# Kernel optimization log

Measured on AMD Instinct MI355X. Metric: run time of the kernel, lower is better.

The kernel has to match this reference:

```python
import jax, jax.numpy as jnp
import numpy as np

# NF4 codebook (16 normal-float levels), same constants as torchao NF4Tensor
NF4_CODEBOOK = jnp.array([
    -1.0, -0.6961928009986877, -0.5250730514526367, -0.39491748809814453,
    -0.28444138169288635, -0.18477343022823334, -0.09105003625154495, 0.0,
    0.07958029955625534, 0.16093020141124725, 0.24611230194568634,
    0.33791524171829224, 0.44070982933044434, 0.5626170039176941,
    0.7229568362236023, 1.0], dtype=jnp.float32)

IN_SIZE = 4096
OUT_SIZE = 12288
BLOCK_SIZE = 64
SCALER_BLOCK_SIZE = 256
EPS = 1e-5


def setup_inputs() -> dict:
    key = jax.random.key(0)
    ks = jax.random.split(key, 7)
    n_blocks = OUT_SIZE * IN_SIZE // BLOCK_SIZE          # 786432
    n_sblocks = n_blocks // SCALER_BLOCK_SIZE            # 3072
    x = jax.random.normal(ks[0], (4096, IN_SIZE), jnp.float32)
    ln_weight = jax.random.uniform(ks[1], (IN_SIZE,), jnp.float32, 0.5, 1.5)
    ln_bias = jax.random.normal(ks[2], (IN_SIZE,), jnp.float32) * 0.02
    codes = jax.random.randint(ks[3], (n_blocks, BLOCK_SIZE), 0, 16, jnp.int32)
    quantized_scalers = jax.random.randint(ks[4], (n_blocks,), 1, 128, jnp.int32)
    quantization_factor = jax.random.uniform(ks[5], (n_sblocks,), jnp.float32, 0.5, 2.0)
    scaler_mean = jax.random.normal(ks[6], (1,), jnp.float32) * 0.01
    return dict(x=x, ln_weight=ln_weight, ln_bias=ln_bias,
                quantization_factor=quantization_factor, scaler_mean=scaler_mean,
                codes=codes, quantized_scalers=quantized_scalers)


def _dequantize_nf4(codes, quantized_scalers, quantization_factor, scaler_mean, in_size):
    # double dequant of per-block scales: int8-range scaler / per-scaler-block factor + mean
    n_blocks = quantized_scalers.shape[0]
    scales = (quantized_scalers.astype(jnp.float32).reshape(-1, SCALER_BLOCK_SIZE)
              / quantization_factor[:, None] + scaler_mean).reshape(n_blocks, 1)
    # codebook lookup + per-block scale, then reshape to [out, in]
    return (NF4_CODEBOOK[codes] * scales).reshape(-1, in_size)


def reference(x, ln_weight, ln_bias, quantization_factor, scaler_mean, codes, quantized_scalers):
    # LayerNorm (eps=1e-5, zero_centered_gamma=False)
    mu = jnp.mean(x, axis=-1, keepdims=True)
    var = jnp.mean(jnp.square(x - mu), axis=-1, keepdims=True)
    ln_out = (x - mu) * jax.lax.rsqrt(var + EPS) * ln_weight + ln_bias
    # NF4 dequant + linear (F.linear: x @ W.T)
    w = _dequantize_nf4(codes, quantized_scalers, quantization_factor, scaler_mean, x.shape[-1])
    linear_out = ln_out @ w.T
    return (linear_out, ln_out)
```

## Files before the change

### kernel.cpp

```cpp
#include <hip/hip_runtime.h>
#include <hip/hip_bf16.h>
#include <stdint.h>

#define IN_SIZE   4096
#define OUT_SIZE  12288
#define M_ROWS    4096
#define LN_EPS    1e-5f
#define N_BLOCKS  786432

typedef __attribute__((ext_vector_type(8))) short bf16x8;
typedef __attribute__((ext_vector_type(4))) float f32x4;

__device__ __constant__ float NF4_CB[16] = {
    -1.0f, -0.6961928009986877f, -0.5250730514526367f, -0.39491748809814453f,
    -0.28444138169288635f, -0.18477343022823334f, -0.09105003625154495f, 0.0f,
    0.07958029955625534f, 0.16093020141124725f, 0.24611230194568634f,
    0.33791524171829224f, 0.44070982933044434f, 0.5626170039176941f,
    0.7229568362236023f, 1.0f };

__device__ __forceinline__ unsigned short f2bf(float f) {
    unsigned u = __builtin_bit_cast(unsigned, f);
    u += 0x7FFFu + ((u >> 16) & 1u);
    return (unsigned short)(u >> 16);
}

__global__ __launch_bounds__(256) void ln_kernel(
    const float* __restrict__ x, const float* __restrict__ gamma,
    const float* __restrict__ beta, float* __restrict__ out_f32,
    unsigned short* __restrict__ out_bf16)
{
    const int row = blockIdx.x;
    const int tid = threadIdx.x;
    const float4* x4 = (const float4*)(x + (size_t)row * IN_SIZE);

    float4 v[4];
    float sum = 0.f, ssq = 0.f;
#pragma unroll
    for (int i = 0; i < 4; ++i) {
        v[i] = x4[tid + i * 256];
        sum += v[i].x + v[i].y + v[i].z + v[i].w;
        ssq += v[i].x * v[i].x + v[i].y * v[i].y + v[i].z * v[i].z + v[i].w * v[i].w;
    }
#pragma unroll
    for (int off = 32; off > 0; off >>= 1) {
        sum += __shfl_down(sum, off, 64);
        ssq += __shfl_down(ssq, off, 64);
    }
    __shared__ float s_sum[4], s_ssq[4];
    const int wave = tid >> 6, lane = tid & 63;
    if (lane == 0) { s_sum[wave] = sum; s_ssq[wave] = ssq; }
    __syncthreads();
    sum = s_sum[0] + s_sum[1] + s_sum[2] + s_sum[3];
    ssq = s_ssq[0] + s_ssq[1] + s_ssq[2] + s_ssq[3];

    const float mu   = sum * (1.f / IN_SIZE);
    const float var  = ssq * (1.f / IN_SIZE) - mu * mu;
    const float rstd = rsqrtf(var + LN_EPS);

    const float4* g4 = (const float4*)gamma;
    const float4* b4 = (const float4*)beta;
    float4* o4 = (float4*)(out_f32 + (size_t)row * IN_SIZE);
    ushort4* ob4 = (ushort4*)(out_bf16 + (size_t)row * IN_SIZE);
#pragma unroll
    for (int i = 0; i < 4; ++i) {
        const int c = tid + i * 256;
        const float4 g = g4[c], b = b4[c];
        float4 y;
        y.x = (v[i].x - mu) * rstd * g.x + b.x;
        y.y = (v[i].y - mu) * rstd * g.y + b.y;
        y.z = (v[i].z - mu) * rstd * g.z + b.z;
        y.w = (v[i].w - mu) * rstd * g.w + b.w;
        o4[c] = y;
        ushort4 p;
        p.x = f2bf(y.x); p.y = f2bf(y.y); p.z = f2bf(y.z); p.w = f2bf(y.w);
        ob4[c] = p;
    }
}

__global__ __launch_bounds__(256) void dq_kernel(
    const int* __restrict__ codes, const int* __restrict__ qs,
    const float* __restrict__ qf, const float* __restrict__ smean,
    unsigned short* __restrict__ wout)
{
    __shared__ float cb[16];
    if (threadIdx.x < 16) cb[threadIdx.x] = NF4_CB[threadIdx.x];
    __syncthreads();

    const size_t t  = (size_t)blockIdx.x * 256 + threadIdx.x;
    const size_t e0 = t * 8;
    const size_t blk = e0 >> 6;
    const float scale = (float)qs[blk] / qf[blk >> 8] + smean[0];

    const int4* c4 = (const int4*)(codes + e0);
    const int4 a = c4[0], b = c4[1];
    ushort4 lo, hi;
    lo.x = f2bf(cb[a.x] * scale); lo.y = f2bf(cb[a.y] * scale);
    lo.z = f2bf(cb[a.z] * scale); lo.w = f2bf(cb[a.w] * scale);
    hi.x = f2bf(cb[b.x] * scale); hi.y = f2bf(cb[b.y] * scale);
    hi.z = f2bf(cb[b.z] * scale); hi.w = f2bf(cb[b.w] * scale);
    *(ushort4*)(wout + e0)     = lo;
    *(ushort4*)(wout + e0 + 4) = hi;
}

#define BKT 64
#define NT  (IN_SIZE / BKT)

#define GL16(src, dst) __builtin_amdgcn_global_load_lds( \
    (const __attribute__((address_space(1))) void*)(src), \
    (__attribute__((address_space(3))) void*)(dst), 16, 0, 0)

template<int QM, int QN>
__device__ __forceinline__ void mmaq(f32x4 (&acc)[8][4],
    const bf16x8 (&a)[4][2], const bf16x8 (&b)[2][2]) {
    __builtin_amdgcn_s_setprio(1);
#pragma unroll
    for (int m = 0; m < 4; ++m)
#pragma unroll
        for (int n = 0; n < 2; ++n)
#pragma unroll
            for (int kk = 0; kk < 2; ++kk)
                acc[QM * 4 + m][QN * 2 + n] = __builtin_amdgcn_mfma_f32_16x16x32_bf16(
                    a[m][kk], b[n][kk], acc[QM * 4 + m][QN * 2 + n], 0, 0, 0);
    __builtin_amdgcn_s_setprio(0);
}

__global__ __launch_bounds__(512, 1) void gemm_kernel(
    const unsigned short* __restrict__ A,
    const unsigned short* __restrict__ B,
    float* __restrict__ C)
{
    extern __shared__ unsigned short lds[];

    const int tid  = threadIdx.x;
    const int lane = tid & 63;
    const int wid  = tid >> 6;
    const int wr   = wid >> 2;
    const int wc   = wid & 3;
    const int fr   = lane & 15, fg = lane >> 4;
    const int frs  = fr & 7;

    constexpr int nwg = (M_ROWS / 256) * (OUT_SIZE / 256);
    const int orig = blockIdx.x;
    const int swz  = (orig & 7) * (nwg >> 3) + (orig >> 3);
    const int tm   = (swz / 96) * 2 + (swz & 1);
    const int tn   = (swz % 96) >> 1;

    const int r0   = tid >> 3;
    const int c8s  = (tid & 7) ^ (r0 & 7);
    const unsigned short* Abase = A + (size_t)(tm * 256 + r0) * IN_SIZE + c8s * 8;
    const unsigned short* Bbase = B + (size_t)(tn * 256 + r0) * IN_SIZE + c8s * 8;

    auto stageA = [&](int T, int h, int buf) {
        const unsigned short* s = Abase + (size_t)h * 128 * IN_SIZE + (size_t)T * 64;
        unsigned short* d = lds + (buf * 2 + h) * 8192 + tid * 8;
        GL16(s, d);
        GL16(s + (size_t)64 * IN_SIZE, d + 4096);
    };
    auto stageB = [&](int T, int h, int buf) {
        const unsigned short* s = Bbase + (size_t)h * 128 * IN_SIZE + (size_t)T * 64;
        unsigned short* d = lds + 32768 + (buf * 2 + h) * 8192 + tid * 8;
        GL16(s, d);
        GL16(s + (size_t)64 * IN_SIZE, d + 4096);
    };
    auto readA = [&](bf16x8 (&a)[4][2], int qm, int buf) {
#pragma unroll
        for (int m = 0; m < 4; ++m)
#pragma unroll
            for (int kk = 0; kk < 2; ++kk)
                a[m][kk] = *(const bf16x8*)(lds + (buf * 2 + wr) * 8192
                                                + (qm * 64 + m * 16 + fr) * 64
                                                + (((kk * 4 + fg) ^ frs) * 8));
    };
    auto readB = [&](bf16x8 (&b)[2][2], int qn, int buf) {
#pragma unroll
        for (int n = 0; n < 2; ++n)
#pragma unroll
            for (int kk = 0; kk < 2; ++kk)
                b[n][kk] = *(const bf16x8*)(lds + 32768 + (buf * 2 + (wc >> 1)) * 8192
                                                + ((wc & 1) * 64 + (qn * 2 + n) * 16 + fr) * 64
                                                + (((kk * 4 + fg) ^ frs) * 8));
    };

    f32x4 acc[8][4] = {};
    bf16x8 a[4][2], a2[4][2], b0A[2][2], b0B[2][2], b1[2][2];

#define TILE_BODY(T, BUF, B0C, B0N, DO_S1, DO_S2, VM, DO_PRE)                 \
    do {                                                                      \
                                                        \
        readA(a, 0, (BUF));                                                   \
        if (DO_S1) stageA((T) + 1, 1, (BUF) ^ 1);                             \
        __builtin_amdgcn_s_barrier();                                         \
        mmaq<0, 0>(acc, a, B0C);                                              \
        __builtin_amdgcn_s_barrier();                                         \
                                                        \
        readB(b1, 1, (BUF));                                                  \
        if (DO_S2) stageB((T) + 2, 0, (BUF));                                 \
        __builtin_amdgcn_s_barrier();                                         \
        mmaq<0, 1>(acc, a, b1);                                               \
        __builtin_amdgcn_s_barrier();                                         \
                                                        \
        readA(a2, 1, (BUF));                                                  \
        if (DO_S2) stageB((T) + 2, 1, (BUF));                                 \
        __builtin_amdgcn_s_barrier();                                         \
        mmaq<1, 0>(acc, a2, B0C);                                             \
        __builtin_amdgcn_s_barrier();                                         \
         \
        if (DO_S2) stageA((T) + 2, 0, (BUF));                                 \
        if ((VM) == 0) asm volatile("s_waitcnt vmcnt(6)" ::: "memory");       \
        else if ((VM) == 1) asm volatile("s_waitcnt vmcnt(0)" ::: "memory");  \
        __builtin_amdgcn_s_barrier();                                         \
        if (DO_PRE) readB(B0N, 0, (BUF) ^ 1);                                 \
        mmaq<1, 1>(acc, a2, b1);                                              \
        __builtin_amdgcn_s_barrier();                                         \
    } while (0)

    stageA(0, 0, 0); stageA(0, 1, 0); stageB(0, 0, 0); stageB(0, 1, 0);
    stageB(1, 0, 1); stageB(1, 1, 1); stageA(1, 0, 1);
    asm volatile("s_waitcnt vmcnt(6)" ::: "memory");
    __builtin_amdgcn_s_barrier();
    readB(b0A, 0, 0);

#pragma unroll 1
    for (int T = 0; T < NT - 2; T += 2) {
        TILE_BODY(T,     0, b0A, b0B, 1, 1, 0, 1);
        TILE_BODY(T + 1, 1, b0B, b0A, 1, 1, 0, 1);
    }
    TILE_BODY(NT - 2, 0, b0A, b0B, 1, 0, 1, 1);
    TILE_BODY(NT - 1, 1, b0B, b0A, 0, 0, 2, 0);
#undef TILE_BODY

    const size_t crow0 = (size_t)(tm * 256 + wr * 128 + fg * 4);
    const int    ccol0 = tn * 256 + wc * 64 + fr;
#pragma unroll
    for (int mg = 0; mg < 8; ++mg)
#pragma unroll
        for (int ng = 0; ng < 4; ++ng)
#pragma unroll
            for (int j = 0; j < 4; ++j)
                C[(crow0 + mg * 16 + j) * OUT_SIZE + ccol0 + ng * 16] = acc[mg][ng][j];
}

extern "C" void kernel_launch(void* const* d_in, const int* in_sizes, int n_in,
                              void* d_out, int out_size, void* d_ws, size_t ws_size,
                              hipStream_t stream) {
    const float* x        = (const float*)d_in[0];
    const float* ln_w     = (const float*)d_in[1];
    const float* ln_b     = (const float*)d_in[2];
    const float* qf       = (const float*)d_in[3];
    const float* smean    = (const float*)d_in[4];
    const int*   codes    = (const int*)d_in[5];
    const int*   qscalers = (const int*)d_in[6];

    float* linear_out = (float*)d_out;
    float* ln_out     = (float*)d_out + (size_t)M_ROWS * OUT_SIZE;

    unsigned short* A_bf16 = (unsigned short*)d_ws;
    unsigned short* W_bf16 = (unsigned short*)((char*)d_ws + (size_t)M_ROWS * IN_SIZE * 2);

    ln_kernel<<<M_ROWS, 256, 0, stream>>>(x, ln_w, ln_b, ln_out, A_bf16);

    const int dq_blocks = (N_BLOCKS * 64 / 8) / 256;
    dq_kernel<<<dq_blocks, 256, 0, stream>>>(codes, qscalers, qf, smean, W_bf16);

    static bool attr_set = false;
    if (!attr_set) {
        (void)hipFuncSetAttribute((const void*)gemm_kernel,
                                  hipFuncAttributeMaxDynamicSharedMemorySize, 131072);
        attr_set = true;
    }
    const int gemm_blocks = (M_ROWS / 256) * (OUT_SIZE / 256);
    gemm_kernel<<<gemm_blocks, 512, 131072, stream>>>(A_bf16, W_bf16, linear_out);
}
```

Measured before the change: 414.5 us.

## Overlap LDS fragment reads with MFMA and halve barriers in GEMM tile loop

Restructures the GEMM main loop so each phase issues the LDS reads for the next MFMA quadrant before running the current quadrant's MFMAs, and prefetches the next tile's A fragment alongside B. This drops the barrier that previously followed each MFMA block, leaving one barrier per phase, and adds sched_barrier fences so the compiler cannot reorder across them. The vmcnt wait moves earlier with a tighter count. The aim is to hide LDS latency and cut synchronization stalls, at the cost of more live registers and a higher risk of LDS read/write races between buffers.

New measurement: 405.6 us. 1.02x faster.

```diff
diff --git a/kernel.cpp b/kernel.cpp
--- a/kernel.cpp
+++ b/kernel.cpp
@@ -109,6 +109,12 @@
     (const __attribute__((address_space(1))) void*)(src), \
     (__attribute__((address_space(3))) void*)(dst), 16, 0, 0)
 
+#define BAR_FENCE() do {                                  \
+    __builtin_amdgcn_s_barrier();                         \
+    __builtin_amdgcn_sched_barrier(0);                    \
+    asm volatile("" ::: "memory");                        \
+} while (0)
+
 template<int QM, int QN>
 __device__ __forceinline__ void mmaq(f32x4 (&acc)[8][4],
     const bf16x8 (&a)[4][2], const bf16x8 (&b)[2][2]) {
@@ -182,42 +188,39 @@
     };
 
     f32x4 acc[8][4] = {};
-    bf16x8 a[4][2], a2[4][2], b0A[2][2], b0B[2][2], b1[2][2];
-
-#define TILE_BODY(T, BUF, B0C, B0N, DO_S1, DO_S2, VM, DO_PRE)                 \
+    bf16x8 a0[4][2], a1[4][2], b0A[2][2], b0B[2][2], b1[2][2];
+
+#define TILE_BODY(T, BUF, B0C, B0N, DO_S1, DO_S2, VM3, DO_PRE)                \
     do {                                                                      \
-                                                        \
-        readA(a, 0, (BUF));                                                   \
+                                                                      \
         if (DO_S1) stageA((T) + 1, 1, (BUF) ^ 1);                             \
-        __builtin_amdgcn_s_barrier();                                         \
-        mmaq<0, 0>(acc, a, B0C);                                              \
-        __builtin_amdgcn_s_barrier();                                         \
-                                                        \
+        BAR_FENCE();                                                          \
         readB(b1, 1, (BUF));                                                  \
+        mmaq<0, 0>(acc, a0, B0C);                                             \
+                                                                      \
         if (DO_S2) stageB((T) + 2, 0, (BUF));                                 \
-        __builtin_amdgcn_s_barrier();                                         \
-        mmaq<0, 1>(acc, a, b1);                                               \
-        __builtin_amdgcn_s_barrier();                                         \
-                                                        \
-        readA(a2, 1, (BUF));                                                  \
+        BAR_FENCE();                                                          \
+        readA(a1, 1, (BUF));                                                  \
+        mmaq<0, 1>(acc, a0, b1);                                              \
+                                                                      \
         if (DO_S2) stageB((T) + 2, 1, (BUF));                                 \
-        __builtin_amdgcn_s_barrier();                                         \
-        mmaq<1, 0>(acc, a2, B0C);                                             \
-        __builtin_amdgcn_s_barrier();                                         \
-         \
+        if ((VM3) == 0) asm volatile("s_waitcnt vmcnt(4)" ::: "memory");      \
+        else if ((VM3) == 1) asm volatile("s_waitcnt vmcnt(0)" ::: "memory"); \
+        BAR_FENCE();                                                          \
+        if (DO_PRE) readA(a0, 0, (BUF) ^ 1);                                  \
+        mmaq<1, 0>(acc, a1, B0C);                                             \
+                                                                      \
         if (DO_S2) stageA((T) + 2, 0, (BUF));                                 \
-        if ((VM) == 0) asm volatile("s_waitcnt vmcnt(6)" ::: "memory");       \
-        else if ((VM) == 1) asm volatile("s_waitcnt vmcnt(0)" ::: "memory");  \
-        __builtin_amdgcn_s_barrier();                                         \
+        BAR_FENCE();                                                          \
         if (DO_PRE) readB(B0N, 0, (BUF) ^ 1);                                 \
-        mmaq<1, 1>(acc, a2, b1);                                              \
-        __builtin_amdgcn_s_barrier();                                         \
+        mmaq<1, 1>(acc, a1, b1);                                              \
     } while (0)
 
     stageA(0, 0, 0); stageA(0, 1, 0); stageB(0, 0, 0); stageB(0, 1, 0);
     stageB(1, 0, 1); stageB(1, 1, 1); stageA(1, 0, 1);
     asm volatile("s_waitcnt vmcnt(6)" ::: "memory");
-    __builtin_amdgcn_s_barrier();
+    BAR_FENCE();
+    readA(a0, 0, 0);
     readB(b0A, 0, 0);
 
 #pragma unroll 1
```
